# Kernel tuning notes

Measured on AMD Instinct MI355X. Metric: run time of the kernel, lower is better.

The kernel has to match this reference:

```python
import jax, jax.numpy as jnp
import numpy as np

INPUT_SIZE = 256
HIDDEN_SIZE = 256


def setup_inputs() -> dict:
    key = jax.random.key(0)
    k_x, k_wxh, k_whh = jax.random.split(key, 3)
    x = jax.random.normal(k_x, (64, 2048, INPUT_SIZE), dtype=jnp.float32)
    # torch nn.Linear weights: [out_features, in_features]
    W_xh = jax.random.normal(k_wxh, (HIDDEN_SIZE, INPUT_SIZE), dtype=jnp.float32) / np.sqrt(INPUT_SIZE)
    W_hh = jax.random.normal(k_whh, (HIDDEN_SIZE, HIDDEN_SIZE), dtype=jnp.float32) / np.sqrt(HIDDEN_SIZE)
    b_h = jnp.zeros((HIDDEN_SIZE,), dtype=jnp.float32)
    return {"x": x, "W_xh": W_xh, "W_hh": W_hh, "b_h": b_h}


def reference(x, W_xh, W_hh, b_h):
    # x: [B, T, D]; h_t = relu(x_t @ W_xh^T + h_{t-1} @ W_hh^T + b_h)
    B, T, _ = x.shape
    # Precompute input projection for all timesteps in one GEMM (same math).
    xproj = jnp.einsum('btd,hd->bth', x, W_xh) + b_h  # [B, T, H]

    def step(h, xp_t):
        h_new = jax.nn.relu(xp_t + h @ W_hh.T)
        return h_new, h_new

    h0 = jnp.zeros((B, HIDDEN_SIZE), dtype=x.dtype)
    # scan over time axis: move T to leading dim
    _, hs = jax.lax.scan(step, h0, jnp.swapaxes(xproj, 0, 1))  # hs: [T, B, H]
    return jnp.swapaxes(hs, 0, 1)  # [B, T, H]
```

## Files before the change

### kernel.cpp

```cpp
#include <hip/hip_runtime.h>

#define BATCH 64
#define SEQT  2048
#define DIM   256
#define HID   256

typedef _Float16 half_t;
typedef _Float16 half2_t __attribute__((ext_vector_type(2)));
typedef _Float16 half4_t __attribute__((ext_vector_type(4)));
typedef _Float16 half8_t __attribute__((ext_vector_type(8)));
typedef float    float4_t __attribute__((ext_vector_type(4)));

__device__ __forceinline__ half8_t cvt8(float4_t a, float4_t b) {
  half8_t r;
  r[0] = (half_t)a[0]; r[1] = (half_t)a[1]; r[2] = (half_t)a[2]; r[3] = (half_t)a[3];
  r[4] = (half_t)b[0]; r[5] = (half_t)b[1]; r[6] = (half_t)b[2]; r[7] = (half_t)b[3];
  return r;
}
#define H2X(v, c) __builtin_shufflevector((v), (v), 2*(c), 2*(c)+1)

template<int CTRL>
__device__ __forceinline__ float dpp_mov(float a) {
  int t = __builtin_amdgcn_mov_dpp(__builtin_bit_cast(int, a), CTRL, 0xF, 0xF, true);
  return __builtin_bit_cast(float, t);
}

#define RNN_BAR() asm volatile("s_waitcnt lgkmcnt(0)\n\ts_barrier" ::: "memory")

__global__ __launch_bounds__(256) void cvt_w_kernel(
    const float* __restrict__ W, half_t* __restrict__ Wh)
{
  const int i = (blockIdx.x * 256 + threadIdx.x) * 4;
  float4_t v = *(const float4_t*)(W + i);
  half4_t o; o[0]=(half_t)v[0]; o[1]=(half_t)v[1]; o[2]=(half_t)v[2]; o[3]=(half_t)v[3];
  *(half4_t*)(Wh + i) = o;
}

__global__ __launch_bounds__(256) void xproj_f16_v2(
    const float* __restrict__ x, const half_t* __restrict__ Wh,
    const float* __restrict__ bh, float* __restrict__ out)
{
  const int lane = threadIdx.x & 63;
  const int wave = threadIdx.x >> 6;
  const int r16  = lane & 15;
  const int kg   = lane >> 4;
  const long m0  = (long)blockIdx.x * 128;

  half8_t bfr[4][8];
  float bb[4];
  #pragma unroll
  for (int qq = 0; qq < 4; ++qq) {
    const int nt = wave * 4 + qq;
    const half_t* wr = Wh + (nt * 16 + r16) * (long)DIM + kg * 8;
    #pragma unroll
    for (int kf = 0; kf < 8; ++kf)
      bfr[qq][kf] = *(const half8_t*)(wr + kf * 32);
    bb[qq] = bh[nt * 16 + r16];
  }
  #pragma unroll 1
  for (int mi = 0; mi < 8; ++mi) {
    const long mrow = m0 + mi * 16;
    half8_t a[8];
    const float* xr = x + (mrow + r16) * (long)DIM + kg * 8;
    #pragma unroll
    for (int kf = 0; kf < 8; ++kf) {
      float4_t x0 = *(const float4_t*)(xr + kf * 32);
      float4_t x1 = *(const float4_t*)(xr + kf * 32 + 4);
      a[kf] = cvt8(x0, x1);
    }
    #pragma unroll
    for (int qq = 0; qq < 4; ++qq) {
      float4_t acc = {bb[qq], bb[qq], bb[qq], bb[qq]};
      #pragma unroll
      for (int kf = 0; kf < 8; ++kf)
        acc = __builtin_amdgcn_mfma_f32_16x16x32_f16(a[kf], bfr[qq][kf], acc, 0, 0, 0);
      float* op = out + (mrow + kg * 4) * (long)HID + (wave * 4 + qq) * 16 + r16;
      #pragma unroll
      for (int r = 0; r < 4; ++r) op[(long)r * HID] = acc[r];
    }
  }
}

__global__ __launch_bounds__(256) void xproj_kernel(
    const float* __restrict__ x, const float* __restrict__ Wxh,
    const float* __restrict__ bh, float* __restrict__ out)
{
  const int lane = threadIdx.x & 63;
  const int wave = threadIdx.x >> 6;
  const int r16  = lane & 15;
  const int kg   = lane >> 4;
  const long m0  = (long)blockIdx.x * 64 + wave * 16;

  half8_t a[8];
  const float* xr = x + (m0 + r16) * (long)DIM + kg * 8;
  #pragma unroll
  for (int kf = 0; kf < 8; ++kf) {
    float4_t x0 = *(const float4_t*)(xr + kf * 32);
    float4_t x1 = *(const float4_t*)(xr + kf * 32 + 4);
    a[kf] = cvt8(x0, x1);
  }
  for (int nt = 0; nt < 16; ++nt) {
    const float* wr = Wxh + (nt * 16 + r16) * (long)DIM + kg * 8;
    float bb = bh[nt * 16 + r16];
    float4_t acc = {bb, bb, bb, bb};
    #pragma unroll
    for (int kf = 0; kf < 8; ++kf) {
      float4_t w0 = *(const float4_t*)(wr + kf * 32);
      float4_t w1 = *(const float4_t*)(wr + kf * 32 + 4);
      acc = __builtin_amdgcn_mfma_f32_16x16x32_f16(a[kf], cvt8(w0, w1), acc, 0, 0, 0);
    }
    float* op = out + (m0 + kg * 4) * (long)HID + nt * 16 + r16;
    #pragma unroll
    for (int r = 0; r < 4; ++r) op[(long)r * HID] = acc[r];
  }
}

#define RNN_STEP(U, XQ)                                                        \
  {                                                                            \
    const int t = t4 + (U);                                                    \
    const int tp = (t + 4 < T) ? (t + 4) : (T - 1);                            \
    float xnew = outp[(long)tp * HID];                                         \
    half8_t hv[4];                                                             \
    _Pragma("unroll")                                                          \
    for (int s = 0; s < 4; ++s)                                                \
      hv[s] = *(const half8_t*)(hraw[(U) & 1] + rb + 16 * s);                  \
    float a0 = 0.f, a1 = 0.f, a2 = 0.f, a3 = 0.f;                              \
    _Pragma("unroll")                                                          \
    for (int s = 0; s < 4; ++s) {                                              \
      a0 = __builtin_amdgcn_fdot2(H2X(w8[0][s], 0), H2X(hv[s], 0), a0, false); \
      a0 = __builtin_amdgcn_fdot2(H2X(w8[0][s], 1), H2X(hv[s], 1), a0, false); \
      a0 = __builtin_amdgcn_fdot2(H2X(w8[0][s], 2), H2X(hv[s], 2), a0, false); \
      a0 = __builtin_amdgcn_fdot2(H2X(w8[0][s], 3), H2X(hv[s], 3), a0, false); \
      a1 = __builtin_amdgcn_fdot2(H2X(w8[1][s], 0), H2X(hv[s], 0), a1, false); \
      a1 = __builtin_amdgcn_fdot2(H2X(w8[1][s], 1), H2X(hv[s], 1), a1, false); \
      a1 = __builtin_amdgcn_fdot2(H2X(w8[1][s], 2), H2X(hv[s], 2), a1, false); \
      a1 = __builtin_amdgcn_fdot2(H2X(w8[1][s], 3), H2X(hv[s], 3), a1, false); \
      a2 = __builtin_amdgcn_fdot2(H2X(w8[2][s], 0), H2X(hv[s], 0), a2, false); \
      a2 = __builtin_amdgcn_fdot2(H2X(w8[2][s], 1), H2X(hv[s], 1), a2, false); \
      a2 = __builtin_amdgcn_fdot2(H2X(w8[2][s], 2), H2X(hv[s], 2), a2, false); \
      a2 = __builtin_amdgcn_fdot2(H2X(w8[2][s], 3), H2X(hv[s], 3), a2, false); \
      a3 = __builtin_amdgcn_fdot2(H2X(w8[3][s], 0), H2X(hv[s], 0), a3, false); \
      a3 = __builtin_amdgcn_fdot2(H2X(w8[3][s], 1), H2X(hv[s], 1), a3, false); \
      a3 = __builtin_amdgcn_fdot2(H2X(w8[3][s], 2), H2X(hv[s], 2), a3, false); \
      a3 = __builtin_amdgcn_fdot2(H2X(w8[3][s], 3), H2X(hv[s], 3), a3, false); \
    }                                                                          \
        \
    float r0 = kA ? a0 : a2;                 \
    float r1 = kA ? a1 : a3;                                                   \
    float b0 = (kA ? a2 : a0) + dpp_mov<0x141>(r0);                            \
    float b1 = (kA ? a3 : a1) + dpp_mov<0x141>(r1);                            \
    float rB = kB ? b0 : b1;                 \
    float c  = (kB ? b1 : b0) + dpp_mov<0x4E>(rB);                             \
    float fin = c + dpp_mov<0xB1>(c);            \
    float y = fmaxf(fin + (XQ), 0.f);                                          \
    outp[(long)t * HID] = y;                                                   \
    *(half_t*)(hraw[((U) & 1) ^ 1] + hwb) = (half_t)y;                         \
    XQ = xnew;                                                                 \
    RNN_BAR();                                                                 \
  }

__global__ __launch_bounds__(512, 1) void rnn_kernel(
    const float* __restrict__ Whh, float* __restrict__ out, int T)
{
  __shared__ alignas(128) unsigned char hraw[2][8 * 80];

  const int tid = threadIdx.x;
  const int l   = tid & 63;
  const int w   = tid >> 6;
  const int g   = l & 7;
  const int j0  = w * 32 + (l >> 3) * 4;
  const int rb  = g * 80;
  const int jown = j0 + ((l >> 1) & 3);
  const int hwb = ((jown >> 5) * 80 + (jown & 31) * 2);
  const bool kA = (l & 4) != 0;
  const bool kB = (l & 2) != 0;
  float* outp = out + (long)blockIdx.x * SEQT * HID + jown;

  half8_t w8[4][4];
  #pragma unroll
  for (int i = 0; i < 4; ++i) {
    const float* wr = Whh + (long)(j0 + i) * HID + g * 32;
    #pragma unroll
    for (int s = 0; s < 4; ++s) {
      float4_t v0 = *(const float4_t*)(wr + s * 8);
      float4_t v1 = *(const float4_t*)(wr + s * 8 + 4);
      w8[i][s] = cvt8(v0, v1);
    }
  }

  if (tid < 160) ((float*)hraw[0])[tid] = 0.f;

  float xq0 = outp[0L * HID];
  float xq1 = outp[1L * HID];
  float xq2 = outp[2L * HID];
  float xq3 = outp[3L * HID];
  RNN_BAR();

  #pragma unroll 1
  for (int t4 = 0; t4 < T; t4 += 4) {
    RNN_STEP(0, xq0)
    RNN_STEP(1, xq1)
    RNN_STEP(2, xq2)
    RNN_STEP(3, xq3)
  }
}

extern "C" void kernel_launch(void* const* d_in, const int* in_sizes, int n_in,
                              void* d_out, int out_size, void* d_ws, size_t ws_size,
                              hipStream_t stream) {
  const float* x   = (const float*)d_in[0];
  const float* Wxh = (const float*)d_in[1];
  const float* Whh = (const float*)d_in[2];
  const float* bh  = (const float*)d_in[3];
  float* out = (float*)d_out;

  if (ws_size >= (size_t)(DIM * HID * sizeof(half_t))) {
    half_t* Wh = (half_t*)d_ws;
    cvt_w_kernel<<<dim3((DIM * HID) / 1024), dim3(256), 0, stream>>>(Wxh, Wh);
    xproj_f16_v2<<<dim3((BATCH * SEQT) / 128), dim3(256), 0, stream>>>(x, Wh, bh, out);
  } else {
    xproj_kernel<<<dim3((BATCH * SEQT) / 64), dim3(256), 0, stream>>>(x, Wxh, bh, out);
  }
  rnn_kernel<<<dim3(BATCH), dim3(512), 0, stream>>>(Whh, out, SEQT);
}
```

Baseline: 940.7 us.

## Fuse input projection and recurrence into one kernel with per-segment flags

Puts the input-projection GEMM and the RNN recurrence into a single launch. Blocks 0-63 run the sequential recurrence chains, and the remaining blocks compute xproj in time segments and publish per-segment ready flags with release atomics. The recurrence blocks poll the flag for the next segment, so the GEMM overlaps the latency-bound recurrence instead of finishing before it starts. The risk is deadlock or stalls if the recurrence blocks occupy CUs before the producer blocks get scheduled, and the polling adds overhead. cvt8 also gains some redundant assignments that have no effect.

```diff
diff --git a/kernel.cpp b/kernel.cpp
--- a/kernel.cpp
+++ b/kernel.cpp
@@ -4,6 +4,8 @@
 #define SEQT  2048
 #define DIM   256
 #define HID   256
+#define NSEG  16
+#define SEGT  128
 
 typedef _Float16 half_t;
 typedef _Float16 half2_t __attribute__((ext_vector_type(2)));
@@ -14,7 +16,9 @@
 __device__ __forceinline__ half8_t cvt8(float4_t a, float4_t b) {
   half8_t r;
   r[0] = (half_t)a[0]; r[1] = (half_t)a[1]; r[2] = (half_t)a[2]; r[3] = (half_t)a[3];
-  r[4] = (half_t)b[0]; r[5] = (half_t)b[1]; r[6] = (half_t)b[2]; r[7] = (half_t)b[3];
+  r[4] = (half_t)b[0]; r[5] = (half_t)b[1]; r[6] = (half_t)b[2]; r[7] = (half_t)b[7-7+4];
+  r[5] = (half_t)b[1]; r[6] = (half_t)b[2]; r[7] = (half_t)b[3];
+  r[4] = (half_t)b[0];
   return r;
 }
 #define H2X(v, c) __builtin_shufflevector((v), (v), 2*(c), 2*(c)+1)
@@ -27,91 +31,27 @@
 
 #define RNN_BAR() asm volatile("s_waitcnt lgkmcnt(0)\n\ts_barrier" ::: "memory")
 
-__global__ __launch_bounds__(256) void cvt_w_kernel(
-    const float* __restrict__ W, half_t* __restrict__ Wh)
+__device__ __forceinline__ void poll_flag(const unsigned int* f) {
+  if (threadIdx.x == 0) {
+    while (__hip_atomic_load(f, __ATOMIC_ACQUIRE, __HIP_MEMORY_SCOPE_AGENT) == 0u)
+      __builtin_amdgcn_s_sleep(2);
+  }
+  __syncthreads();
+}
+
+__global__ __launch_bounds__(256) void prep_kernel(
+    const float* __restrict__ W, half_t* __restrict__ Wh,
+    unsigned int* __restrict__ flags)
 {
   const int i = (blockIdx.x * 256 + threadIdx.x) * 4;
   float4_t v = *(const float4_t*)(W + i);
   half4_t o; o[0]=(half_t)v[0]; o[1]=(half_t)v[1]; o[2]=(half_t)v[2]; o[3]=(half_t)v[3];
   *(half4_t*)(Wh + i) = o;
-}
-
-__global__ __launch_bounds__(256) void xproj_f16_v2(
-    const float* __restrict__ x, const half_t* __restrict__ Wh,
-    const float* __restrict__ bh, float* __restrict__ out)
-{
-  const int lane = threadIdx.x & 63;
-  const int wave = threadIdx.x >> 6;
-  const int r16  = lane & 15;
-  const int kg   = lane >> 4;
-  const long m0  = (long)blockIdx.x * 128;
-
-  half8_t bfr[4][8];
-  float bb[4];
-  #pragma unroll
-  for (int qq = 0; qq < 4; ++qq) {
-    const int nt = wave * 4 + qq;
-    const half_t* wr = Wh + (nt * 16 + r16) * (long)DIM + kg * 8;
-    #pragma unroll
-    for (int kf = 0; kf < 8; ++kf)
-      bfr[qq][kf] = *(const half8_t*)(wr + kf * 32);
-    bb[qq] = bh[nt * 16 + r16];
-  }
-  #pragma unroll 1
-  for (int mi = 0; mi < 8; ++mi) {
-    const long mrow = m0 + mi * 16;
-    half8_t a[8];
-    const float* xr = x + (mrow + r16) * (long)DIM + kg * 8;
-    #pragma unroll
-    for (int kf = 0; kf < 8; ++kf) {
-      float4_t x0 = *(const float4_t*)(xr + kf * 32);
-      float4_t x1 = *(const float4_t*)(xr + kf * 32 + 4);
-      a[kf] = cvt8(x0, x1);
-    }
-    #pragma unroll
-    for (int qq = 0; qq < 4; ++qq) {
-      float4_t acc = {bb[qq], bb[qq], bb[qq], bb[qq]};
-      #pragma unroll
-      for (int kf = 0; kf < 8; ++kf)
-        acc = __builtin_amdgcn_mfma_f32_16x16x32_f16(a[kf], bfr[qq][kf], acc, 0, 0, 0);
-      float* op = out + (mrow + kg * 4) * (long)HID + (wave * 4 + qq) * 16 + r16;
-      #pragma unroll
-      for (int r = 0; r < 4; ++r) op[(long)r * HID] = acc[r];
-    }
-  }
-}
-
-__global__ __launch_bounds__(256) void xproj_kernel(
-    const float* __restrict__ x, const float* __restrict__ Wxh,
-    const float* __restrict__ bh, float* __restrict__ out)
-{
-  const int lane = threadIdx.x & 63;
-  const int wave = threadIdx.x >> 6;
-  const int r16  = lane & 15;
-  const int kg   = lane >> 4;
-  const long m0  = (long)blockIdx.x * 64 + wave * 16;
-
-  half8_t a[8];
-  const float* xr = x + (m0 + r16) * (long)DIM + kg * 8;
-  #pragma unroll
-  for (int kf = 0; kf < 8; ++kf) {
-    float4_t x0 = *(const float4_t*)(xr + kf * 32);
-    float4_t x1 = *(const float4_t*)(xr + kf * 32 + 4);
-    a[kf] = cvt8(x0, x1);
-  }
-  for (int nt = 0; nt < 16; ++nt) {
-    const float* wr = Wxh + (nt * 16 + r16) * (long)DIM + kg * 8;
-    float bb = bh[nt * 16 + r16];
-    float4_t acc = {bb, bb, bb, bb};
-    #pragma unroll
-    for (int kf = 0; kf < 8; ++kf) {
-      float4_t w0 = *(const float4_t*)(wr + kf * 32);
-      float4_t w1 = *(const float4_t*)(wr + kf * 32 + 4);
-      acc = __builtin_amdgcn_mfma_f32_16x16x32_f16(a[kf], cvt8(w0, w1), acc, 0, 0, 0);
-    }
-    float* op = out + (m0 + kg * 4) * (long)HID + nt * 16 + r16;
-    #pragma unroll
-    for (int r = 0; r < 4; ++r) op[(long)r * HID] = acc[r];
+  if (blockIdx.x == 0) {
+    flags[threadIdx.x]       = 0u;
+    flags[threadIdx.x + 256] = 0u;
+    flags[threadIdx.x + 512] = 0u;
+    flags[threadIdx.x + 768] = 0u;
   }
 }
 
@@ -144,20 +84,160 @@
       a3 = __builtin_amdgcn_fdot2(H2X(w8[3][s], 2), H2X(hv[s], 2), a3, false); \
       a3 = __builtin_amdgcn_fdot2(H2X(w8[3][s], 3), H2X(hv[s], 3), a3, false); \
     }                                                                          \
-        \
-    float r0 = kA ? a0 : a2;                 \
+    float r0 = kA ? a0 : a2;                                                   \
     float r1 = kA ? a1 : a3;                                                   \
     float b0 = (kA ? a2 : a0) + dpp_mov<0x141>(r0);                            \
     float b1 = (kA ? a3 : a1) + dpp_mov<0x141>(r1);                            \
-    float rB = kB ? b0 : b1;                 \
+    float rB = kB ? b0 : b1;                                                   \
     float c  = (kB ? b1 : b0) + dpp_mov<0x4E>(rB);                             \
-    float fin = c + dpp_mov<0xB1>(c);            \
+    float fin = c + dpp_mov<0xB1>(c);                                          \
     float y = fmaxf(fin + (XQ), 0.f);                                          \
     outp[(long)t * HID] = y;                                                   \
     *(half_t*)(hraw[((U) & 1) ^ 1] + hwb) = (half_t)y;                         \
     XQ = xnew;                                                                 \
     RNN_BAR();                                                                 \
   }
+
+__global__ __launch_bounds__(512, 1) void fused_kernel(
+    const float* __restrict__ x, const half_t* __restrict__ Wxh16,
+    const float* __restrict__ Whh, const float* __restrict__ bh,
+    float* __restrict__ out, unsigned int* __restrict__ flags, int T)
+{
+  if (blockIdx.x >= 64) {
+    const int b = blockIdx.x - 64;
+    const int k = b >> 6;
+    const int c = b & 63;
+    const int lane = threadIdx.x & 63;
+    const int w = threadIdx.x >> 6;
+    const int r16 = lane & 15;
+    const int kg = lane >> 4;
+    const long m0 = ((long)c * NSEG + k) * SEGT;
+
+    half8_t bfr[2][8];
+    float bb[2];
+    #pragma unroll
+    for (int i = 0; i < 2; ++i) {
+      const int nt = w * 2 + i;
+      const half_t* wr = Wxh16 + (nt * 16 + r16) * (long)DIM + kg * 8;
+      #pragma unroll
+      for (int kf = 0; kf < 8; ++kf)
+        bfr[i][kf] = *(const half8_t*)(wr + kf * 32);
+      bb[i] = bh[nt * 16 + r16];
+    }
+    #pragma unroll 1
+    for (int mi = 0; mi < 8; ++mi) {
+      const long mrow = m0 + mi * 16;
+      half8_t a[8];
+      const float* xr = x + (mrow + r16) * (long)DIM + kg * 8;
+      #pragma unroll
+      for (int kf = 0; kf < 8; ++kf) {
+        float4_t x0 = *(const float4_t*)(xr + kf * 32);
+        float4_t x1 = *(const float4_t*)(xr + kf * 32 + 4);
+        a[kf] = cvt8(x0, x1);
+      }
+      #pragma unroll
+      for (int i = 0; i < 2; ++i) {
+        float4_t acc = {bb[i], bb[i], bb[i], bb[i]};
+        #pragma unroll
+        for (int kf = 0; kf < 8; ++kf)
+          acc = __builtin_amdgcn_mfma_f32_16x16x32_f16(a[kf], bfr[i][kf], acc, 0, 0, 0);
+        float* op = out + (mrow + kg * 4) * (long)HID + (w * 2 + i) * 16 + r16;
+        #pragma unroll
+        for (int r = 0; r < 4; ++r) op[(long)r * HID] = acc[r];
+      }
+    }
+    __syncthreads();
+    if (threadIdx.x == 0)
+      __hip_atomic_store(flags + ((c << 4) | k), 1u, __ATOMIC_RELEASE,
+                         __HIP_MEMORY_SCOPE_AGENT);
+    return;
+  }
+
+  __shared__ alignas(128) unsigned char hraw[2][8 * 80];
+
+  const int chain = blockIdx.x;
+  const int tid = threadIdx.x;
+  const int l   = tid & 63;
+  const int w   = tid >> 6;
+  const int g   = l & 7;
+  const int j0  = w * 32 + (l >> 3) * 4;
+  const int rb  = g * 80;
+  const int jown = j0 + ((l >> 1) & 3);
+  const int hwb = ((jown >> 5) * 80 + (jown & 31) * 2);
+  const bool kA = (l & 4) != 0;
+  const bool kB = (l & 2) != 0;
+  const unsigned int* fl = flags + (chain << 4);
+  float* outp = out + (long)chain * SEQT * HID + jown;
+
+  half8_t w8[4][4];
+  #pragma unroll
+  for (int i = 0; i < 4; ++i) {
+    const float* wr = Whh + (long)(j0 + i) * HID + g * 32;
+    #pragma unroll
+    for (int s = 0; s < 4; ++s) {
+      float4_t v0 = *(const float4_t*)(wr + s * 8);
+      float4_t v1 = *(const float4_t*)(wr + s * 8 + 4);
+      w8[i][s] = cvt8(v0, v1);
+    }
+  }
+
+  if (tid < 160) ((float*)hraw[0])[tid] = 0.f;
+
+  poll_flag(fl + 0);
+  float xq0 = outp[0L * HID];
+  float xq1 = outp[1L * HID];
+  float xq2 = outp[2L * HID];
+  float xq3 = outp[3L * HID];
+  RNN_BAR();
+
+  #pragma unroll 1
+  for (int seg = 0; seg < NSEG; ++seg) {
+    const int ps = (seg + 1 < NSEG) ? (seg + 1) : (NSEG - 1);
+    poll_flag(fl + ps);
+    const int tend = seg * SEGT + SEGT;
+    #pragma unroll 1
+    for (int t4 = seg * SEGT; t4 < tend; t4 += 4) {
+      RNN_STEP(0, xq0)
+      RNN_STEP(1, xq1)
+      RNN_STEP(2, xq2)
+      RNN_STEP(3, xq3)
+    }
+  }
+}
+
+__global__ __launch_bounds__(256) void xproj_kernel(
+    const float* __restrict__ x, const float* __restrict__ Wxh,
+    const float* __restrict__ bh, float* __restrict__ out)
+{
+  const int lane = threadIdx.x & 63;
+  const int wave = threadIdx.x >> 6;
+  const int r16  = lane & 15;
+  const int kg   = lane >> 4;
+  const long m0  = (long)blockIdx.x * 64 + wave * 16;
+
+  half8_t a[8];
+  const float* xr = x + (m0 + r16) * (long)DIM + kg * 8;
+  #pragma unroll
+  for (int kf = 0; kf < 8; ++kf) {
+    float4_t x0 = *(const float4_t*)(xr + kf * 32);
+    float4_t x1 = *(const float4_t*)(xr + kf * 32 + 4);
+    a[kf] = cvt8(x0, x1);
+  }
+  for (int nt = 0; nt < 16; ++nt) {
+    const float* wr = Wxh + (nt * 16 + r16) * (long)DIM + kg * 8;
+    float bb = bh[nt * 16 + r16];
+    float4_t acc = {bb, bb, bb, bb};
+    #pragma unroll
+    for (int kf = 0; kf < 8; ++kf) {
+      float4_t w0 = *(const float4_t*)(wr + kf * 32);
+      float4_t w1 = *(const float4_t*)(wr + kf * 32 + 4);
+      acc = __builtin_amdgcn_mfma_f32_16x16x32_f16(a[kf], cvt8(w0, w1), acc, 0, 0, 0);
+    }
+    float* op = out + (m0 + kg * 4) * (long)HID + nt * 16 + r16;
+    #pragma unroll
+    for (int r = 0; r < 4; ++r) op[(long)r * HID] = acc[r];
+  }
+}
 
 __global__ __launch_bounds__(512, 1) void rnn_kernel(
     const float* __restrict__ Whh, float* __restrict__ out, int T)
@@ -187,7 +267,6 @@
       w8[i][s] = cvt8(v0, v1);
     }
   }
-
   if (tid < 160) ((float*)hraw[0])[tid] = 0.f;
 
   float xq0 = outp[0L * HID];
@@ -214,12 +293,17 @@
   const float* bh  = (const float*)d_in[3];
   float* out = (float*)d_out;
 
-  if (ws_size >= (size_t)(DIM * HID * sizeof(half_t))) {
+  const size_t wh_bytes = (size_t)DIM * HID * sizeof(half_t);
+  const size_t need = wh_bytes + 4096;
+
+  if (ws_size >= need) {
     half_t* Wh = (half_t*)d_ws;
-    cvt_w_kernel<<<dim3((DIM * HID) / 1024), dim3(256), 0, stream>>>(Wxh, Wh);
-    xproj_f16_v2<<<dim3((BATCH * SEQT) / 128), dim3(256), 0, stream>>>(x, Wh, bh, out);
+    unsigned int* flags = (unsigned int*)((char*)d_ws + wh_bytes);
+    prep_kernel<<<dim3((DIM * HID) / 1024), dim3(256), 0, stream>>>(Wxh, Wh, flags);
+    fused_kernel<<<dim3(64 + BATCH * NSEG), dim3(512), 0, stream>>>(
+        x, Wh, Whh, bh, out, flags, SEQT);
   } else {
     xproj_kernel<<<dim3((BATCH * SEQT) / 64), dim3(256), 0, stream>>>(x, Wxh, bh, out);
-  }
-  rnn_kernel<<<dim3(BATCH), dim3(512), 0, stream>>>(Whh, out, SEQT);
-}
+    rnn_kernel<<<dim3(BATCH), dim3(512), 0, stream>>>(Whh, out, SEQT);
+  }
+}
```

Result: faster. 891.1 us (-5.3%).
